# Kernel optimization log

Measured on AMD Instinct MI355X. Metric: run time of the kernel, lower is better.

Reference implementation:

```python
import jax, jax.numpy as jnp
import numpy as np

PI = 3.1415  # matches the literal constant in the source


def setup_inputs() -> dict:
    key = jax.random.key(0)
    nt, ns, nh = 1024, 2048, 32
    k1, k2, k3, k4, k5 = jax.random.split(key, 5)
    P = jax.random.uniform(k1, (nt, ns), dtype=jnp.float32) * 10.0           # precipitation >= 0
    T1 = jax.random.normal(k2, (nt, ns), dtype=jnp.float32) * 10.0           # daily min temp
    T2 = T1 + jax.random.uniform(k3, (nt, ns), dtype=jnp.float32) * 15.0 + 0.5  # max temp > min temp
    E = jax.random.uniform(k4, (nt, ns), dtype=jnp.float32) * 5.0            # potential ET >= 0
    w = jax.random.uniform(k5, (nh * 4,), dtype=jnp.float32, minval=-1.0, maxval=1.0)
    return {"P": P, "T1": T1, "T2": T2, "E": E, "w": w}


def reference(P, T1, T2, E, w):
    nt, ns = P.shape
    nh = w.shape[0] // 4

    # rain/snow partition. arccos argument is clipped for numerical safety; the
    # clipped region (|ratio|>1) is exactly where rP is overwritten by the masks,
    # so forward values match the original exactly.
    Ta = (T1 + T2) * 0.5
    ratio = jnp.clip((T1 + T2) / (T2 - T1), -1.0, 1.0)
    rP = 1.0 - jnp.arccos(ratio) / PI
    rP = jnp.where(T1 >= 0, 1.0, rP)
    rP = jnp.where(T2 <= 0, 0.0, rP)
    Ps = (1.0 - rP) * P   # snow
    Pl = rP * P           # liquid rain

    gm = jnp.exp(w[:nh]) + 1.0            # melt factor, [nh]
    ge = jax.nn.sigmoid(w[nh:2 * nh])     # ET gate, [nh]
    go = jax.nn.sigmoid(w[2 * nh:3 * nh]) # outflow gate, [nh]
    ga = jax.nn.softmax(w[3 * nh:])       # mixing weights (Dropout in eval mode = identity), [nh]

    def step(carry, xs):
        S0, H0 = carry                    # each [ns, nh]
        Ta_k, Ps_k, Pl_k, E_k = xs        # each [ns]
        Sm = jnp.minimum(S0, jnp.maximum(Ta_k[:, None] * gm, 0.0))  # snowmelt
        S = S0 + Ps_k[:, None]
        H = jnp.maximum(H0 + Sm + Pl_k[:, None] - E_k[:, None] * ge, 0.0)
        Q = H * go
        Y = jnp.sum(Q * ga, axis=1)       # [ns]
        return (S - Sm, H - Q), Y

    init = (jnp.zeros((ns, nh), P.dtype), jnp.zeros((ns, nh), P.dtype))
    _, Yout = jax.lax.scan(step, init, (Ta, Ps, Pl, E))
    return Yout  # [nt, ns]
```

## Files before the change

### kernel.cpp

```cpp
#include <hip/hip_runtime.h>

#define NT 1024
#define NS 2048
#define NH 32

__global__ __launch_bounds__(256, 1)
void waternet_kernel(const float* __restrict__ P,
                     const float* __restrict__ T1,
                     const float* __restrict__ T2,
                     const float* __restrict__ E,
                     const float* __restrict__ w,
                     float* __restrict__ Y)
{
    const int tid  = threadIdx.x;
    const int lane = tid & 31;
    const int grp  = tid >> 5;

    const int bid    = blockIdx.x;
    const int sChunk = (bid & 7) * 32 + (bid >> 3);
    const int s      = sChunk * 8 + grp;

    const float wm = w[lane];
    const float we = w[NH + lane];
    const float wo = w[2 * NH + lane];
    const float wa = w[3 * NH + lane];

    const float gm = expf(wm) + 1.0f;
    const float ge = 1.0f / (1.0f + expf(-we));
    const float go = 1.0f / (1.0f + expf(-wo));

    float mx = wa;
    #pragma unroll
    for (int o = 16; o; o >>= 1) mx = fmaxf(mx, __shfl_xor(mx, o));
    float ea = expf(wa - mx);
    float ssum = ea;
    #pragma unroll
    for (int o = 16; o; o >>= 1) ssum += __shfl_xor(ssum, o);
    const float ga  = ea / ssum;
    const float go1 = 1.0f - go;
    const float gq  = go * ga;

    float S  = 0.0f;
    float Hs = 0.0f;

    __shared__ float4 stage[8][32];
    __shared__ float  ytmp[8][32][33];

    size_t base = (size_t)lane * NS + s;
    float p0 = P[base], a0 = T1[base], b0 = T2[base], e0 = E[base];

    for (int c = 0; c < 32; ++c) {
        const float p = p0, ta = a0, tb = b0, ee = e0;
        if (c < 31) {
            size_t nb = base + (size_t)(c + 1) * 32 * NS;
            p0 = P[nb]; a0 = T1[nb]; b0 = T2[nb]; e0 = E[nb];
        }

        float sum   = ta + tb;
        float diff  = tb - ta;
        float ratio = sum / diff;
        ratio = fminf(fmaxf(ratio, -1.0f), 1.0f);
        float rP = 1.0f - acosf(ratio) * (1.0f / 3.1415f);
        if (ta >= 0.0f) rP = 1.0f;
        if (tb <= 0.0f) rP = 0.0f;
        const float Pl  = rP * p;
        const float Ps  = p - Pl;
        const float TaP = fmaxf(sum * 0.5f, 0.0f);
        stage[grp][lane] = make_float4(TaP, Ps, Pl, ee);

        #pragma unroll
        for (int k = 0; k < 32; ++k) {
            const float4 x  = stage[grp][k];
            const float bm  = x.x * gm;
            const float Sm  = fminf(S, bm);
            const float add = x.z + Sm;
            const float h3  = fmaxf(fmaf(-x.w, ge, Hs + add), 0.0f);
            S  = (S + x.y) - Sm;
            Hs = h3 * go1;
            ytmp[grp][k][lane] = h3 * gq;
        }

        float a0s = 0.0f, a1s = 0.0f, a2s = 0.0f, a3s = 0.0f;
        #pragma unroll
        for (int k = 0; k < 32; k += 4) {
            a0s += ytmp[grp][lane][k + 0];
            a1s += ytmp[grp][lane][k + 1];
            a2s += ytmp[grp][lane][k + 2];
            a3s += ytmp[grp][lane][k + 3];
        }
        Y[(size_t)(c * 32 + lane) * NS + s] = (a0s + a1s) + (a2s + a3s);
    }
}

extern "C" void kernel_launch(void* const* d_in, const int* in_sizes, int n_in,
                              void* d_out, int out_size, void* d_ws, size_t ws_size,
                              hipStream_t stream) {
    const float* P  = (const float*)d_in[0];
    const float* T1 = (const float*)d_in[1];
    const float* T2 = (const float*)d_in[2];
    const float* E  = (const float*)d_in[3];
    const float* w  = (const float*)d_in[4];
    float* Y = (float*)d_out;

    waternet_kernel<<<dim3(256), dim3(256), 0, stream>>>(P, T1, T2, E, w, Y);
}
```

Measured before the change: 53.93 us.

## Double-buffer staged inputs and software-pipeline LDS reads in the recurrence

```diff
diff --git a/kernel.cpp b/kernel.cpp
--- a/kernel.cpp
+++ b/kernel.cpp
@@ -3,6 +3,7 @@
 #define NT 1024
 #define NS 2048
 #define NH 32
+#define PF 8
 
 __global__ __launch_bounds__(256, 1)
 void waternet_kernel(const float* __restrict__ P,
@@ -43,52 +44,75 @@
     float S  = 0.0f;
     float Hs = 0.0f;
 
-    __shared__ float4 stage[8][32];
+    __shared__ float4 stage[2][8][32];
     __shared__ float  ytmp[8][32][33];
 
     size_t base = (size_t)lane * NS + s;
     float p0 = P[base], a0 = T1[base], b0 = T2[base], e0 = E[base];
+    size_t bn = base + (size_t)32 * NS;
+    float pg = P[bn], ag = T1[bn], bg = T2[bn], eg = E[bn];
 
-    for (int c = 0; c < 32; ++c) {
-        const float p = p0, ta = a0, tb = b0, ee = e0;
-        if (c < 31) {
-            size_t nb = base + (size_t)(c + 1) * 32 * NS;
-            p0 = P[nb]; a0 = T1[nb]; b0 = T2[nb]; e0 = E[nb];
-        }
-
+    auto prep = [&](float p, float ta, float tb, float ee, int buf) {
         float sum   = ta + tb;
-        float diff  = tb - ta;
-        float ratio = sum / diff;
+        float ratio = sum / (tb - ta);
         ratio = fminf(fmaxf(ratio, -1.0f), 1.0f);
         float rP = 1.0f - acosf(ratio) * (1.0f / 3.1415f);
         if (ta >= 0.0f) rP = 1.0f;
         if (tb <= 0.0f) rP = 0.0f;
-        const float Pl  = rP * p;
-        const float Ps  = p - Pl;
-        const float TaP = fmaxf(sum * 0.5f, 0.0f);
-        stage[grp][lane] = make_float4(TaP, Ps, Pl, ee);
+        float Pl  = rP * p;
+        float Ps  = p - Pl;
+        float TaP = fmaxf(sum * 0.5f, 0.0f);
+        stage[buf][grp][lane] = make_float4(TaP, Ps, Pl, ee);
+    };
+
+    prep(p0, a0, b0, e0, 0);
+
+    float xx[PF], xy[PF], xw[PF];
+    #pragma unroll
+    for (int j = 0; j < PF; ++j) {
+        float4 x = stage[0][grp][j];
+        xx[j] = x.x * gm;
+        xy[j] = x.y;
+        xw[j] = x.z - x.w * ge;
+    }
+
+    #pragma unroll 2
+    for (int c = 0; c < 32; ++c) {
+        if (c < 31) prep(pg, ag, bg, eg, (c + 1) & 1);
+        if (c < 30) {
+            size_t nb = base + (size_t)(c + 2) * 32 * NS;
+            pg = P[nb]; ag = T1[nb]; bg = T2[nb]; eg = E[nb];
+        }
 
         #pragma unroll
         for (int k = 0; k < 32; ++k) {
-            const float4 x  = stage[grp][k];
-            const float bm  = x.x * gm;
-            const float Sm  = fminf(S, bm);
-            const float add = x.z + Sm;
-            const float h3  = fmaxf(fmaf(-x.w, ge, Hs + add), 0.0f);
-            S  = (S + x.y) - Sm;
+            const int sl = k & (PF - 1);
+            const float bm = xx[sl], Ps = xy[sl], pw = xw[sl];
+            const float Sm = fminf(S, bm);
+            const float t  = Hs + pw;
+            const float Sn = (S + Ps) - Sm;
+            const float h3 = fmaxf(t + Sm, 0.0f);
+            S  = Sn;
             Hs = h3 * go1;
             ytmp[grp][k][lane] = h3 * gq;
+
+            const int idx = k + PF;
+            const int buf = (c + (idx >> 5)) & 1;
+            float4 x = stage[buf][grp][idx & 31];
+            xx[sl] = x.x * gm;
+            xy[sl] = x.y;
+            xw[sl] = x.z - x.w * ge;
         }
 
-        float a0s = 0.0f, a1s = 0.0f, a2s = 0.0f, a3s = 0.0f;
+        float r0 = 0.f, r1 = 0.f, r2 = 0.f, r3 = 0.f;
         #pragma unroll
         for (int k = 0; k < 32; k += 4) {
-            a0s += ytmp[grp][lane][k + 0];
-            a1s += ytmp[grp][lane][k + 1];
-            a2s += ytmp[grp][lane][k + 2];
-            a3s += ytmp[grp][lane][k + 3];
+            r0 += ytmp[grp][lane][k + 0];
+            r1 += ytmp[grp][lane][k + 1];
+            r2 += ytmp[grp][lane][k + 2];
+            r3 += ytmp[grp][lane][k + 3];
         }
-        Y[(size_t)(c * 32 + lane) * NS + s] = (a0s + a1s) + (a2s + a3s);
+        Y[(size_t)(c * 32 + lane) * NS + s] = (r0 + r1) + (r2 + r3);
     }
 }
 
```

Measured after the change: 47.75 us. 1.13x faster.
